# Kernel tuning notes

Measured on AMD Instinct MI355X. Metric: run time of the kernel, lower is better.

Reference implementation:

```python
import jax, jax.numpy as jnp
import numpy as np

INPUT_DIM = 28
OUTPUT_DIM = 21
LAYER_SIZE = 64
NUM_HIDDEN = 10  # number of 64x64 hidden layers after the input layer


def setup_inputs() -> dict:
    key = jax.random.key(0)
    ks = jax.random.split(key, 7)
    x = jax.random.normal(ks[0], (1048576, INPUT_DIM), dtype=jnp.float32)
    # PyTorch nn.Linear default init: U(-1/sqrt(fan_in), 1/sqrt(fan_in)); plain uniform is fine for a baseline.
    s_in = 1.0 / np.sqrt(INPUT_DIM)
    s_h = 1.0 / np.sqrt(LAYER_SIZE)
    W_in = jax.random.uniform(ks[1], (INPUT_DIM, LAYER_SIZE), jnp.float32, -s_in, s_in)
    b_in = jax.random.uniform(ks[2], (LAYER_SIZE,), jnp.float32, -s_in, s_in)
    W_hid = jax.random.uniform(ks[3], (NUM_HIDDEN, LAYER_SIZE, LAYER_SIZE), jnp.float32, -s_h, s_h)
    b_hid = jax.random.uniform(ks[4], (NUM_HIDDEN, LAYER_SIZE), jnp.float32, -s_h, s_h)
    W_out = jax.random.uniform(ks[5], (LAYER_SIZE, OUTPUT_DIM), jnp.float32, -s_h, s_h)
    b_out = jax.random.uniform(ks[6], (OUTPUT_DIM,), jnp.float32, -s_h, s_h)
    return {"x": x, "W_in": W_in, "b_in": b_in, "W_hid": W_hid, "b_hid": b_hid,
            "W_out": W_out, "b_out": b_out}


def reference(x, W_in, b_in, W_hid, b_hid, W_out, b_out):
    h = jax.nn.relu(x @ W_in + b_in)  # [B, 64]
    def step(h, wb):
        W, b = wb
        return jax.nn.relu(h @ W + b), None
    h, _ = jax.lax.scan(step, h, (W_hid, b_hid))
    return jax.nn.sigmoid(h @ W_out + b_out)  # [B, 21]
```

## Files before the change

kernel.cpp:

```cpp
#include <hip/hip_runtime.h>

#define DEV __device__ __forceinline__

typedef _Float16 half8 __attribute__((ext_vector_type(8)));
typedef _Float16 half2v __attribute__((ext_vector_type(2)));
typedef float f32x16 __attribute__((ext_vector_type(16)));
typedef int int4v __attribute__((ext_vector_type(4)));

DEV f32x16 mfma16(half8 a, half8 b, f32x16 c) {
    return __builtin_amdgcn_mfma_f32_32x32x16_f16(a, b, c, 0, 0, 0);
}
DEV half8 h8(int4v v) { return __builtin_bit_cast(half8, v); }
DEV int pkrtz(float a, float b) {
    auto t = __builtin_amdgcn_cvt_pkrtz(a, b);
    return __builtin_bit_cast(int, t);
}
DEV int relupk(float a, float b) {
    int p = pkrtz(a, b);
    half2v h = __builtin_bit_cast(half2v, p);
    half2v z = {(_Float16)0.f, (_Float16)0.f};
    h = __builtin_elementwise_max(h, z);
    return __builtin_bit_cast(int, h);
}
DEV void plswap(int& a, int& b) {
    asm("v_permlane32_swap_b32 %0, %1" : "+v"(a), "+v"(b));
}

DEV f32x16 zero16() {
    f32x16 z = {0.f,0.f,0.f,0.f,0.f,0.f,0.f,0.f,0.f,0.f,0.f,0.f,0.f,0.f,0.f,0.f};
    return z;
}

struct Frags { int4v c[4]; };

DEV void repack(const f32x16& C0, const f32x16& C1, Frags& B) {
    int P0[8], P1[8];
#pragma unroll
    for (int q = 0; q < 8; ++q) {
        P0[q] = relupk(C0[2*q], C0[2*q+1]);
        P1[q] = relupk(C1[2*q], C1[2*q+1]);
    }
#pragma unroll
    for (int kk = 0; kk < 4; ++kk) {
        const int* Pm = (kk < 2) ? P0 : P1;
        int idx = 4 * (kk & 1);
        int a0 = Pm[idx + 0], b0 = Pm[idx + 2];
        int a1 = Pm[idx + 1], b1 = Pm[idx + 3];
        plswap(a0, b0);
        plswap(a1, b1);
        int4v nb; nb[0] = a0; nb[1] = a1; nb[2] = b0; nb[3] = b1;
        B.c[kk] = nb;
    }
}

DEV void hid_proc(const half8* A0, const half8* A1, int4v ones, Frags& B) {
    f32x16 C0 = mfma16(A0[4], h8(ones), zero16());
    f32x16 C1 = mfma16(A1[4], h8(ones), zero16());
#pragma unroll
    for (int kk = 0; kk < 4; ++kk) {
        half8 bf = h8(B.c[kk]);
        C0 = mfma16(A0[kk], bf, C0);
        C1 = mfma16(A1[kk], bf, C1);
    }
    repack(C0, C1, B);
}

DEV void hid_step(const _Float16* wb, int lam, int4v ones, Frags& B0, Frags& B1) {
    half8 A0[5], A1[5];
#pragma unroll
    for (int kk = 0; kk < 5; ++kk) {
        A0[kk] = *(const half8*)(wb + kk * 512 + lam * 8);
        A1[kk] = *(const half8*)(wb + 2560 + kk * 512 + lam * 8);
    }
    hid_proc(A0, A1, ones, B0);
    hid_proc(A0, A1, ones, B1);
}

DEV void in_step(const _Float16* wb, int lam, Frags& B0, Frags& B1) {
    half8 A0[2], A1[2];
#pragma unroll
    for (int kk = 0; kk < 2; ++kk) {
        A0[kk] = *(const half8*)(wb + kk * 512 + lam * 8);
        A1[kk] = *(const half8*)(wb + 1024 + kk * 512 + lam * 8);
    }
    {
        f32x16 C0 = mfma16(A0[0], h8(B0.c[0]), zero16());
        f32x16 C1 = mfma16(A1[0], h8(B0.c[0]), zero16());
        C0 = mfma16(A0[1], h8(B0.c[1]), C0);
        C1 = mfma16(A1[1], h8(B0.c[1]), C1);
        repack(C0, C1, B0);
    }
    {
        f32x16 C0 = mfma16(A0[0], h8(B1.c[0]), zero16());
        f32x16 C1 = mfma16(A1[0], h8(B1.c[0]), zero16());
        C0 = mfma16(A0[1], h8(B1.c[1]), C0);
        C1 = mfma16(A1[1], h8(B1.c[1]), C1);
        repack(C0, C1, B1);
    }
}

DEV void out_step2(const _Float16* wb, int lam, int4v ones,
                   const Frags& B0, const Frags& B1, float* __restrict__ out, int row0, int row1) {
    const int h = lam >> 5;
    half8 A[5];
#pragma unroll
    for (int kk = 0; kk < 5; ++kk) A[kk] = *(const half8*)(wb + kk * 512 + lam * 8);
    f32x16 Ca = mfma16(A[4], h8(ones), zero16());
    f32x16 Cb = mfma16(A[4], h8(ones), zero16());
#pragma unroll
    for (int kk = 0; kk < 4; ++kk) {
        Ca = mfma16(A[kk], h8(B0.c[kk]), Ca);
        Cb = mfma16(A[kk], h8(B1.c[kk]), Cb);
    }
    float* oa = out + row0 * 21;
    float* ob = out + row1 * 21;
#pragma unroll
    for (int r = 0; r < 16; ++r) {
        int f = (r & 3) + 8 * (r >> 2) + 4 * h;
        if (f < 21) {
            oa[f] = __builtin_amdgcn_rcpf(1.f + __expf(-Ca[r]));
            ob[f] = __builtin_amdgcn_rcpf(1.f + __expf(-Cb[r]));
        }
    }
}

DEV void load_x(const float* __restrict__ x, int row, int h, Frags& B) {
    const float* xr = x + row * 28;
    float4 fa = *(const float4*)(xr + 8 * h);
    float4 fb = *(const float4*)(xr + 8 * h + 4);
    float4 fc = *(const float4*)(xr + 16 + 8 * h);
    float4 fd = (h == 0) ? *(const float4*)(xr + 20) : make_float4(1.f, 0.f, 0.f, 0.f);
    int4v c0, c1;
    c0[0] = pkrtz(fa.x, fa.y); c0[1] = pkrtz(fa.z, fa.w);
    c0[2] = pkrtz(fb.x, fb.y); c0[3] = pkrtz(fb.z, fb.w);
    c1[0] = pkrtz(fc.x, fc.y); c1[1] = pkrtz(fc.z, fc.w);
    c1[2] = pkrtz(fd.x, fd.y); c1[3] = pkrtz(fd.z, fd.w);
    B.c[0] = c0; B.c[1] = c1;
}

#define NT 1024

__global__ __attribute__((amdgpu_flat_work_group_size(NT, NT), amdgpu_waves_per_eu(4, 4)))
void mlp_fused(
    const float* __restrict__ x, const float* __restrict__ W_in, const float* __restrict__ b_in,
    const float* __restrict__ W_hid, const float* __restrict__ b_hid,
    const float* __restrict__ W_out, const float* __restrict__ b_out,
    float* __restrict__ out) {
    __shared__ __align__(16) _Float16 wH[51200];
    __shared__ __align__(16) _Float16 wI[2048];
    __shared__ __align__(16) _Float16 wO[2560];

    const int tid = threadIdx.x;

    for (int i = tid; i < 10240; i += NT) {
        int l = i >> 10, rem = i & 1023, m = rem >> 9, off = rem & 511;
        wH[l * 5120 + m * 2560 + 2048 + off] = (_Float16)0.f;
    }
    for (int i = tid; i < 2048; i += NT) wI[i] = (_Float16)0.f;
    for (int i = tid; i < 2560; i += NT) wO[i] = (_Float16)0.f;
    __syncthreads();

    for (int i = tid; i < 40960; i += NT) {
        int o = i & 63, kin = (i >> 6) & 63, l = i >> 12;
        int m = o >> 5, kk = kin >> 4, hh = (kin >> 3) & 1, e = kin & 7;
        int lam = hh * 32 + (o & 31);
        wH[l * 5120 + m * 2560 + kk * 512 + lam * 8 + e] = (_Float16)W_hid[i];
    }
    for (int i = tid; i < 640; i += NT) {
        int l = i >> 6, f = i & 63, m = f >> 5, r = f & 31;
        wH[l * 5120 + m * 2560 + 2048 + r * 8] = (_Float16)b_hid[i];
    }
    for (int i = tid; i < 1792; i += NT) {
        int o = i & 63, kin = i >> 6;
        int m = o >> 5, kk = kin >> 4, hh = (kin >> 3) & 1, e = kin & 7;
        int lam = hh * 32 + (o & 31);
        wI[m * 1024 + kk * 512 + lam * 8 + e] = (_Float16)W_in[i];
    }
    for (int i = tid; i < 64; i += NT) {
        int m = i >> 5;
        wI[m * 1024 + 512 + (32 + (i & 31)) * 8 + 4] = (_Float16)b_in[i];
    }
    for (int i = tid; i < 1344; i += NT) {
        int o = i % 21, kin = i / 21;
        int kk = kin >> 4, hh = (kin >> 3) & 1, e = kin & 7;
        int lam = hh * 32 + o;
        wO[kk * 512 + lam * 8 + e] = (_Float16)W_out[i];
    }
    for (int i = tid; i < 21; i += NT)
        wO[4 * 512 + i * 8] = (_Float16)b_out[i];
    __syncthreads();

    const int w = tid >> 6, lam = tid & 63;
    const int col = lam & 31, h = lam >> 5;
    int4v ones; ones[0] = (h == 0) ? 0x3C00 : 0; ones[1] = 0; ones[2] = 0; ones[3] = 0;

    const int tbase = blockIdx.x * 128;
#pragma unroll 1
    for (int pb = w * 2; pb < 128; pb += 32) {
        int t0 = tbase + pb;
        int row0 = t0 * 32 + col, row1 = row0 + 32;
        Frags B0, B1;
        load_x(x, row0, h, B0);
        load_x(x, row1, h, B1);
        in_step(wI, lam, B0, B1);
        const _Float16* wp = wH;
#pragma unroll 1
        for (int l = 0; l < 10; ++l) {
            hid_step(wp, lam, ones, B0, B1);
            wp += 5120;
        }
        out_step2(wO, lam, ones, B0, B1, out, row0, row1);
    }
}

extern "C" void kernel_launch(void* const* d_in, const int* in_sizes, int n_in,
                              void* d_out, int out_size, void* d_ws, size_t ws_size,
                              hipStream_t stream) {
    const float* x     = (const float*)d_in[0];
    const float* W_in  = (const float*)d_in[1];
    const float* b_in  = (const float*)d_in[2];
    const float* W_hid = (const float*)d_in[3];
    const float* b_hid = (const float*)d_in[4];
    const float* W_out = (const float*)d_in[5];
    const float* b_out = (const float*)d_in[6];
    float* out = (float*)d_out;
    mlp_fused<<<dim3(256), dim3(NT), 0, stream>>>(x, W_in, b_in, W_hid, b_hid, W_out, b_out, out);
}
```

Baseline: 118.5 us.

## Double-buffer hidden-layer weight loads and halve block size with wave staggering

The hidden-layer loop now prefetches the next layer's weight fragments from LDS into registers while the current layer's MFMAs run, two layers per iteration. The LDS buffer is padded by one extra layer so the final prefetch stays in bounds. Input and output layer weights are loaded into registers once, MFMAs are wrapped in s_setprio, and odd waves are staggered with s_sleep so matrix and VALU phases of different waves overlap. The block shrinks to 512 threads at 2 waves per EU, which gives each thread more registers for the extra buffers but halves the number of resident waves available to hide latency.

```diff
diff --git a/kernel.cpp b/kernel.cpp
--- a/kernel.cpp
+++ b/kernel.cpp
@@ -11,6 +11,7 @@
     return __builtin_amdgcn_mfma_f32_32x32x16_f16(a, b, c, 0, 0, 0);
 }
 DEV half8 h8(int4v v) { return __builtin_bit_cast(half8, v); }
+DEV half8 ldh8(const _Float16* p) { return *(const half8*)p; }
 DEV int pkrtz(float a, float b) {
     auto t = __builtin_amdgcn_cvt_pkrtz(a, b);
     return __builtin_bit_cast(int, t);
@@ -53,65 +54,63 @@
     }
 }
 
-DEV void hid_proc(const half8* A0, const half8* A1, int4v ones, Frags& B) {
-    f32x16 C0 = mfma16(A0[4], h8(ones), zero16());
-    f32x16 C1 = mfma16(A1[4], h8(ones), zero16());
+DEV void loadA5(const _Float16* base, int lam, half8* A0, half8* A1) {
+    const _Float16* p0 = base + lam * 8;
+    const _Float16* p1 = base + 2560 + lam * 8;
+#pragma unroll
+    for (int kk = 0; kk < 5; ++kk) {
+        A0[kk] = ldh8(p0 + kk * 512);
+        A1[kk] = ldh8(p1 + kk * 512);
+    }
+}
+
+DEV void step2(const half8* A0, const half8* A1, int4v ones, Frags& B0, Frags& B1) {
+    __builtin_amdgcn_s_setprio(1);
+    f32x16 C00 = mfma16(A0[4], h8(ones), zero16());
+    f32x16 C01 = mfma16(A1[4], h8(ones), zero16());
+    f32x16 C10 = mfma16(A0[4], h8(ones), zero16());
+    f32x16 C11 = mfma16(A1[4], h8(ones), zero16());
 #pragma unroll
     for (int kk = 0; kk < 4; ++kk) {
-        half8 bf = h8(B.c[kk]);
-        C0 = mfma16(A0[kk], bf, C0);
-        C1 = mfma16(A1[kk], bf, C1);
-    }
-    repack(C0, C1, B);
-}
-
-DEV void hid_step(const _Float16* wb, int lam, int4v ones, Frags& B0, Frags& B1) {
-    half8 A0[5], A1[5];
-#pragma unroll
-    for (int kk = 0; kk < 5; ++kk) {
-        A0[kk] = *(const half8*)(wb + kk * 512 + lam * 8);
-        A1[kk] = *(const half8*)(wb + 2560 + kk * 512 + lam * 8);
-    }
-    hid_proc(A0, A1, ones, B0);
-    hid_proc(A0, A1, ones, B1);
-}
-
-DEV void in_step(const _Float16* wb, int lam, Frags& B0, Frags& B1) {
-    half8 A0[2], A1[2];
-#pragma unroll
-    for (int kk = 0; kk < 2; ++kk) {
-        A0[kk] = *(const half8*)(wb + kk * 512 + lam * 8);
-        A1[kk] = *(const half8*)(wb + 1024 + kk * 512 + lam * 8);
-    }
-    {
-        f32x16 C0 = mfma16(A0[0], h8(B0.c[0]), zero16());
-        f32x16 C1 = mfma16(A1[0], h8(B0.c[0]), zero16());
-        C0 = mfma16(A0[1], h8(B0.c[1]), C0);
-        C1 = mfma16(A1[1], h8(B0.c[1]), C1);
-        repack(C0, C1, B0);
-    }
-    {
-        f32x16 C0 = mfma16(A0[0], h8(B1.c[0]), zero16());
-        f32x16 C1 = mfma16(A1[0], h8(B1.c[0]), zero16());
-        C0 = mfma16(A0[1], h8(B1.c[1]), C0);
-        C1 = mfma16(A1[1], h8(B1.c[1]), C1);
-        repack(C0, C1, B1);
-    }
-}
-
-DEV void out_step2(const _Float16* wb, int lam, int4v ones,
-                   const Frags& B0, const Frags& B1, float* __restrict__ out, int row0, int row1) {
+        half8 b0 = h8(B0.c[kk]);
+        half8 b1 = h8(B1.c[kk]);
+        C00 = mfma16(A0[kk], b0, C00);
+        C01 = mfma16(A1[kk], b0, C01);
+        C10 = mfma16(A0[kk], b1, C10);
+        C11 = mfma16(A1[kk], b1, C11);
+    }
+    __builtin_amdgcn_s_setprio(0);
+    repack(C00, C01, B0);
+    repack(C10, C11, B1);
+}
+
+DEV void in_step(const half8* I0, const half8* I1, Frags& B0, Frags& B1) {
+    __builtin_amdgcn_s_setprio(1);
+    f32x16 C00 = mfma16(I0[0], h8(B0.c[0]), zero16());
+    f32x16 C01 = mfma16(I1[0], h8(B0.c[0]), zero16());
+    f32x16 C10 = mfma16(I0[0], h8(B1.c[0]), zero16());
+    f32x16 C11 = mfma16(I1[0], h8(B1.c[0]), zero16());
+    C00 = mfma16(I0[1], h8(B0.c[1]), C00);
+    C01 = mfma16(I1[1], h8(B0.c[1]), C01);
+    C10 = mfma16(I0[1], h8(B1.c[1]), C10);
+    C11 = mfma16(I1[1], h8(B1.c[1]), C11);
+    __builtin_amdgcn_s_setprio(0);
+    repack(C00, C01, B0);
+    repack(C10, C11, B1);
+}
+
+DEV void out_step(const half8* Ao, int lam, int4v ones,
+                  const Frags& B0, const Frags& B1, float* __restrict__ out, int row0, int row1) {
     const int h = lam >> 5;
-    half8 A[5];
-#pragma unroll
-    for (int kk = 0; kk < 5; ++kk) A[kk] = *(const half8*)(wb + kk * 512 + lam * 8);
-    f32x16 Ca = mfma16(A[4], h8(ones), zero16());
-    f32x16 Cb = mfma16(A[4], h8(ones), zero16());
+    __builtin_amdgcn_s_setprio(1);
+    f32x16 Ca = mfma16(Ao[4], h8(ones), zero16());
+    f32x16 Cb = mfma16(Ao[4], h8(ones), zero16());
 #pragma unroll
     for (int kk = 0; kk < 4; ++kk) {
-        Ca = mfma16(A[kk], h8(B0.c[kk]), Ca);
-        Cb = mfma16(A[kk], h8(B1.c[kk]), Cb);
-    }
+        Ca = mfma16(Ao[kk], h8(B0.c[kk]), Ca);
+        Cb = mfma16(Ao[kk], h8(B1.c[kk]), Cb);
+    }
+    __builtin_amdgcn_s_setprio(0);
     float* oa = out + row0 * 21;
     float* ob = out + row1 * 21;
 #pragma unroll
@@ -138,15 +137,15 @@
     B.c[0] = c0; B.c[1] = c1;
 }
 
-#define NT 1024
-
-__global__ __attribute__((amdgpu_flat_work_group_size(NT, NT), amdgpu_waves_per_eu(4, 4)))
+#define NT 512
+
+__global__ __attribute__((amdgpu_flat_work_group_size(NT, NT), amdgpu_waves_per_eu(2, 2)))
 void mlp_fused(
     const float* __restrict__ x, const float* __restrict__ W_in, const float* __restrict__ b_in,
     const float* __restrict__ W_hid, const float* __restrict__ b_hid,
     const float* __restrict__ W_out, const float* __restrict__ b_out,
     float* __restrict__ out) {
-    __shared__ __align__(16) _Float16 wH[51200];
+    __shared__ __align__(16) _Float16 wH[56320];
     __shared__ __align__(16) _Float16 wI[2048];
     __shared__ __align__(16) _Float16 wO[2560];
 
@@ -194,22 +193,44 @@
     const int col = lam & 31, h = lam >> 5;
     int4v ones; ones[0] = (h == 0) ? 0x3C00 : 0; ones[1] = 0; ones[2] = 0; ones[3] = 0;
 
+    half8 I0[2], I1[2], Ao[5];
+    {
+        const _Float16* p0 = wI + lam * 8;
+        const _Float16* p1 = wI + 1024 + lam * 8;
+#pragma unroll
+        for (int kk = 0; kk < 2; ++kk) {
+            I0[kk] = ldh8(p0 + kk * 512);
+            I1[kk] = ldh8(p1 + kk * 512);
+        }
+        const _Float16* po = wO + lam * 8;
+#pragma unroll
+        for (int kk = 0; kk < 5; ++kk) Ao[kk] = ldh8(po + kk * 512);
+    }
+
+    if (w & 1) __builtin_amdgcn_s_sleep(13);
+
     const int tbase = blockIdx.x * 128;
 #pragma unroll 1
-    for (int pb = w * 2; pb < 128; pb += 32) {
-        int t0 = tbase + pb;
+    for (int j = 0; j < 8; ++j) {
+        int p = w * 8 + j;
+        int t0 = tbase + p * 2;
         int row0 = t0 * 32 + col, row1 = row0 + 32;
         Frags B0, B1;
         load_x(x, row0, h, B0);
         load_x(x, row1, h, B1);
-        in_step(wI, lam, B0, B1);
-        const _Float16* wp = wH;
+        half8 Aa0[5], Aa1[5], Ab0[5], Ab1[5];
+        loadA5(wH, lam, Aa0, Aa1);
+        in_step(I0, I1, B0, B1);
+        const _Float16* base = wH;
 #pragma unroll 1
-        for (int l = 0; l < 10; ++l) {
-            hid_step(wp, lam, ones, B0, B1);
-            wp += 5120;
+        for (int l2 = 0; l2 < 5; ++l2) {
+            loadA5(base + 5120, lam, Ab0, Ab1);
+            step2(Aa0, Aa1, ones, B0, B1);
+            loadA5(base + 10240, lam, Aa0, Aa1);
+            step2(Ab0, Ab1, ones, B0, B1);
+            base += 10240;
         }
-        out_step2(wO, lam, ones, B0, B1, out, row0, row1);
+        out_step(Ao, lam, ones, B0, B1, out, row0, row1);
     }
 }
 
```

After: 123.0 us. +3.7%, slower.
